# Optimization experiments

Measured on AMD Instinct MI355X. Metric: run time of the kernel, lower is better.

Reference implementation:

```python
import jax, jax.numpy as jnp
import numpy as np


def _conv_same(x, w):
    # NHWC input, HWIO kernel, stride 1, SAME padding
    return jax.lax.conv_general_dilated(
        x, w, window_strides=(1, 1), padding='SAME',
        dimension_numbers=('NHWC', 'HWIO', 'NHWC'))


def _maxpool2(x):
    return jax.lax.reduce_window(
        x, -jnp.inf, jax.lax.max,
        window_dimensions=(1, 2, 2, 1), window_strides=(1, 2, 2, 1),
        padding='VALID')


def _binarize(x):
    # sign binarization with straight-through estimator (XNOR-net / Riptide)
    return x + jax.lax.stop_gradient(jnp.sign(x) - x)


def _binary_conv_relu(x, w):
    # BinaryConv2D: binarize activations and weights, conv, relu, no bias
    return jax.nn.relu(_conv_same(_binarize(x), _binarize(w)))


def setup_inputs() -> dict:
    key = jax.random.key(0)
    ks = jax.random.split(key, 32)
    d = {}
    d['x'] = jax.random.normal(ks[0], (128, 32, 32, 3), dtype=jnp.float32)
    d['w1'] = jax.random.normal(ks[1], (3, 3, 3, 128), dtype=jnp.float32) * 0.1
    d['b1'] = jax.random.normal(ks[2], (128,), dtype=jnp.float32) * 0.1
    chans = [128, 128, 256, 256, 512, 512]
    kshapes = [(3, 3, 128, 128), (3, 3, 128, 256), (3, 3, 256, 256),
               (3, 3, 256, 512), (3, 3, 512, 512)]
    for i, shp in zip(range(2, 7), kshapes):
        d[f'w{i}'] = jax.random.normal(ks[2 + i], shp, dtype=jnp.float32) * 0.1
    for i in range(1, 7):
        c = chans[i - 1]
        d[f'bn{i}_scale'] = jax.random.uniform(ks[10 + i], (c,), dtype=jnp.float32, minval=0.5, maxval=1.5)
        d[f'bn{i}_bias'] = jax.random.normal(ks[20 + i], (c,), dtype=jnp.float32) * 0.1
    d['dense_w'] = jax.random.normal(ks[30], (512, 10), dtype=jnp.float32) * 0.05
    d['dense_b'] = jax.random.normal(ks[31], (10,), dtype=jnp.float32) * 0.05
    return d


def reference(x, w1, b1, bn1_scale, bn1_bias, w2, bn2_scale, bn2_bias,
              w3, bn3_scale, bn3_bias, w4, bn4_scale, bn4_bias,
              w5, bn5_scale, bn5_bias, w6, bn6_scale, bn6_bias,
              dense_w, dense_b):
    # conv1: normal float conv + relu, then BN (inference: fused scale/bias)
    h = jax.nn.relu(_conv_same(x, w1) + b1)
    h = h * bn1_scale + bn1_bias
    # conv2 (binary) -> pool -> bn2
    h = _binary_conv_relu(h, w2)
    h = _maxpool2(h)
    h = h * bn2_scale + bn2_bias
    # conv3 (binary) -> bn3
    h = _binary_conv_relu(h, w3)
    h = h * bn3_scale + bn3_bias
    # conv4 (binary) -> pool -> bn4
    h = _binary_conv_relu(h, w4)
    h = _maxpool2(h)
    h = h * bn4_scale + bn4_bias
    # conv5 (binary) -> bn5
    h = _binary_conv_relu(h, w5)
    h = h * bn5_scale + bn5_bias
    # conv6 (binary) -> pool -> bn6
    h = _binary_conv_relu(h, w6)
    h = _maxpool2(h)  # -> [B, 4, 4, 512]
    h = h * bn6_scale + bn6_bias
    # Dense applied on last axis (original code has no flatten): [B,4,4,10]
    logits = jnp.einsum('bhwc,cd->bhwd', h, dense_w) + dense_b
    return jax.nn.softmax(logits, axis=-1)
```

## Files before the change

### kernel.cpp

```cpp
#include <hip/hip_runtime.h>
#include <cstdint>
#include <math.h>

typedef unsigned long long u64;


__global__ void zero_kernel(u64* __restrict__ p, int n) {
    int i = blockIdx.x * blockDim.x + threadIdx.x;
    int stride = gridDim.x * blockDim.x;
    for (; i < n; i += stride) p[i] = 0;
}

__global__ __launch_bounds__(256) void pack_kernel(
        const float* __restrict__ w2, const float* __restrict__ w3,
        const float* __restrict__ w4, const float* __restrict__ w5,
        const float* __restrict__ w6,
        u64* __restrict__ wq2, u64* __restrict__ wq3, u64* __restrict__ wq4,
        u64* __restrict__ wq5, u64* __restrict__ wq6) {
    int wid = (blockIdx.x * 256 + threadIdx.x) >> 6;
    int lane = threadIdx.x & 63;
    const float* w; u64* wq; int Wi, Cout, base;
    if      (wid <  2304) { w = w2; wq = wq2; Wi = 2; Cout = 128; base = 0; }
    else if (wid <  6912) { w = w3; wq = wq3; Wi = 2; Cout = 256; base = 2304; }
    else if (wid < 16128) { w = w4; wq = wq4; Wi = 4; Cout = 256; base = 6912; }
    else if (wid < 34560) { w = w5; wq = wq5; Wi = 4; Cout = 512; base = 16128; }
    else if (wid < 71424) { w = w6; wq = wq6; Wi = 8; Cout = 512; base = 34560; }
    else return;
    int id = wid - base;
    int oc = id % Cout;
    int tw = id / Cout;
    int tap = tw / Wi, cw = tw % Wi;
    int Cin = Wi * 64;
    float v = w[((size_t)tap * Cin + cw * 64 + lane) * Cout + oc];
    u64 mask = __ballot(!(v > 0.0f));
    if (lane == 0) wq[((size_t)oc * Wi + cw) * 9 + tap] = mask;
}

__global__ __launch_bounds__(256) void meta_kernel(
        const u64* __restrict__ wq2, const u64* __restrict__ wq3,
        const u64* __restrict__ wq4, const u64* __restrict__ wq5,
        const u64* __restrict__ wq6,
        const float* s2, const float* b2, const float* s3, const float* b3,
        const float* s4, const float* b4, const float* s5, const float* b5,
        const float* s6, const float* b6,
        int* __restrict__ mt) {
    int wid = (blockIdx.x * 256 + threadIdx.x) >> 6;
    int lane = threadIdx.x & 63;
    if (wid >= 1664) return;
    const u64* wq; int WI, oc, mbase; const float* sc; const float* bi;
    if      (wid <  128) { wq = wq2; WI = 2; oc = wid;        mbase = 0;     sc = s2; bi = b2; }
    else if (wid <  384) { wq = wq3; WI = 2; oc = wid - 128;  mbase = 1536;  sc = s3; bi = b3; }
    else if (wid <  640) { wq = wq4; WI = 4; oc = wid - 384;  mbase = 4608;  sc = s4; bi = b4; }
    else if (wid < 1152) { wq = wq5; WI = 4; oc = wid - 640;  mbase = 7680;  sc = s5; bi = b5; }
    else                 { wq = wq6; WI = 8; oc = wid - 1152; mbase = 13824; sc = s6; bi = b6; }
    int P = 0;
    if (lane < 9) {
        int s = 0;
        for (int cw = 0; cw < WI; cw++)
            s += (int)__popcll(wq[((size_t)oc * WI + cw) * 9 + lane]);
        P = 64 * WI - s;
    }
    int p0 = __shfl(P, 0, 64), p1 = __shfl(P, 1, 64), p2 = __shfl(P, 2, 64);
    int p3 = __shfl(P, 3, 64), p5 = __shfl(P, 5, 64);
    int p6 = __shfl(P, 6, 64), p7 = __shfl(P, 7, 64), p8 = __shfl(P, 8, 64);
    if (lane == 0) {
        int* mo = mt + mbase + oc * 12;
        mo[0] = p0 + p1 + p2;
        mo[1] = p6 + p7 + p8;
        mo[2] = p0 + p3 + p6;
        mo[3] = p2 + p5 + p8;
        mo[4] = p0; mo[5] = p2; mo[6] = p6; mo[7] = p8;
        double tneg = -(double)bi[oc] / (double)sc[oc];
        mo[8] = (tneg < 0.0) ? -(1 << 29) : (int)floor(tneg);
    }
}

__global__ __launch_bounds__(128) void conv1_pack_kernel(
        const float* __restrict__ x, const float* __restrict__ w1,
        const float* __restrict__ b1, const float* __restrict__ s1,
        const float* __restrict__ bb1, u64* __restrict__ p1) {
    const int t = threadIdx.x;
    const int oc = t;
    const int bx = blockIdx.x;
    const int xseg = (bx & 3) << 3;
    const int y = (bx >> 2) & 31;
    const int b = bx >> 7;

    double wreg[27];
    #pragma unroll
    for (int k = 0; k < 27; k++) wreg[k] = (double)w1[k * 128 + oc];
    const double b1v = (double)b1[oc];
    const double tneg = -(double)bb1[oc] / (double)s1[oc];
    const bool always = tneg < 0.0;
    const double thr = tneg - b1v;

    double acc[8];
    #pragma unroll
    for (int i = 0; i < 8; i++) acc[i] = 0.0;

    #pragma unroll
    for (int ky = 0; ky < 3; ky++) {
        int iy = y - 1 + ky;
        if (iy < 0 || iy > 31) continue;
        #pragma unroll
        for (int col = 0; col < 10; col++) {
            int ix = xseg - 1 + col;
            if (ix < 0 || ix > 31) continue;
            const float* xp = x + ((b * 32 + iy) * 32 + ix) * 3;
            #pragma unroll
            for (int c = 0; c < 3; c++) {
                double xv = (double)xp[c];
                #pragma unroll
                for (int kx = 0; kx < 3; kx++) {
                    int px = col - kx;
                    if (px >= 0 && px < 8)
                        acc[px] += xv * wreg[(ky * 3 + kx) * 3 + c];
                }
            }
        }
    }
    const int w = t >> 6;
    #pragma unroll
    for (int px = 0; px < 8; px++) {
        bool bit = always || (acc[px] > thr);
        u64 m = __ballot(bit);
        if ((t & 63) == 0)
            p1[(((size_t)w * 128 + b) * 34 + y + 1) * 34 + xseg + px + 1] = m;
    }
}

template<int WI, int H, int W, int COUT, bool POOL, int OCG, bool BITOUT>
__global__ __launch_bounds__(256, 4) void bconv6_kernel(
        const u64* __restrict__ in, const u64* __restrict__ wq,
        const int* __restrict__ mt,
        const float* __restrict__ bns, const float* __restrict__ bnb,
        u64* __restrict__ outb, float* __restrict__ outf) {
    constexpr int Hp = H + 2, Wp = W + 2;
    constexpr int Ho = POOL ? H / 2 : H;
    constexpr int Wo = POOL ? W / 2 : W;
    constexpr int TX = W / 8;
    constexpr int TILES = (H / 8) * (W / 8);
    constexpr int NG = COUT / OCG;

    const int lane = threadIdx.x & 63;
    int wid = (blockIdx.x * blockDim.x + threadIdx.x) >> 6;
    wid = __builtin_amdgcn_readfirstlane(wid);
    const int g = wid % NG;
    int tb = wid / NG;
    const int tile = tb % TILES;
    const int b = tb / TILES;
    if (b >= 128) return;
    const int ly = lane >> 3, lx = lane & 7;
    const int py = (tile / TX) * 8 + ly;
    const int px = (tile % TX) * 8 + lx;
    const int oc0 = g * OCG;

    const int ft = (py == 0), fb = (py == H - 1);
    const int fl = (px == 0), fr = (px == W - 1);
    const int ctl = ft & fl, ctr = ft & fr, cbl = fb & fl, cbr = fb & fr;
    const int n_oob = 3 * (ft + fb + fl + fr) - ctl - ctr - cbl - cbr;
    const int dbase = -64 * WI * (9 + n_oob);
    const bool anyedge = __ballot(ft | fb | fl | fr) != 0;

    int m[OCG];
    #pragma unroll
    for (int o = 0; o < OCG; o++) m[o] = 0;

    const u64* ab = in + ((size_t)b * Hp + py) * Wp + px;
    const u64* wb0 = wq + (size_t)oc0 * WI * 9;

    #pragma unroll 1
    for (int cw = 0; cw < WI; cw++) {
        const u64* ap = ab + (size_t)cw * (128 * Hp * Wp);
        u64 act[9];
        #pragma unroll
        for (int ky = 0; ky < 3; ky++)
            #pragma unroll
            for (int kx = 0; kx < 3; kx++)
                act[ky * 3 + kx] = ap[ky * Wp + kx];
        const u64* wb = wb0 + (size_t)cw * 9;
        #pragma unroll
        for (int o = 0; o < OCG; o++) {
            const u64* wl = wb + (size_t)o * (WI * 9);
            int a0 = m[o], a1 = 0, a2 = 0, a3 = 0;
            #pragma unroll
            for (int t9 = 0; t9 < 9; t9++) {
                u64 xo = act[t9] ^ wl[t9];
                int lo = __builtin_popcount((unsigned)xo);
                int hi = __builtin_popcount((unsigned)(xo >> 32));
                if (t9 & 1) { a1 = lo + a1; a3 = hi + a3; }
                else        { a0 = lo + a0; a2 = hi + a2; }
            }
            m[o] = (a0 + a2) + (a1 + a3);
        }
    }

    const bool master = POOL ? (((ly | lx) & 1) == 0) : true;
    const int opy = POOL ? (py >> 1) : py, opx = POOL ? (px >> 1) : px;
    unsigned mask = 0;

    #pragma unroll
    for (int o = 0; o < OCG; o++) {
        const int* mo = mt + (size_t)(oc0 + o) * 12;
        int d;
        if (anyedge) {
            int S = ft * mo[0] + fb * mo[1] + fl * mo[2] + fr * mo[3]
                  - ctl * mo[4] - ctr * mo[5] - cbl * mo[6] - cbr * mo[7];
            d = 2 * (m[o] + S) + dbase;
        } else {
            d = 2 * m[o] - 64 * WI * 9;
        }
        if constexpr (BITOUT) {
            mask |= (unsigned)(d > mo[8]) << o;
        } else {
            int dm = max(d, __shfl_xor(d, 1, 64));
            int dp = max(dm, __shfl_xor(dm, 8, 64));
            int pmax = dp > 0 ? dp : 0;
            float h = (float)pmax * bns[oc0 + o] + bnb[oc0 + o];
            if (master)
                outf[(size_t)((b * 4 + opy) * 4 + opx) * 512 + oc0 + o] = h;
        }
    }

    if constexpr (BITOUT) {
        if constexpr (POOL) {
            mask |= __shfl_xor(mask, 1, 64);
            mask |= __shfl_xor(mask, 8, 64);
        }
        if (master) {
            size_t idx = (((size_t)(oc0 >> 6) * 128 + b) * (Ho + 2) + opy + 1)
                         * (Wo + 2) + opx + 1;
            char* bp = (char*)(outb + idx) + ((oc0 & 63) >> 3);
            if constexpr (OCG == 32) *(unsigned*)bp = mask;
            else *(unsigned short*)bp = (unsigned short)mask;
        }
    }
}

__global__ __launch_bounds__(256) void dense_softmax_kernel(
        const float* __restrict__ h6, const float* __restrict__ dw,
        const float* __restrict__ db, float* __restrict__ out) {
    int lane = threadIdx.x & 63;
    int r = (blockIdx.x * blockDim.x + threadIdx.x) >> 6;
    if (r >= 2048) return;
    const float* hr = h6 + (size_t)r * 512;
    float part[10];
    #pragma unroll
    for (int d = 0; d < 10; d++) part[d] = 0.f;
    #pragma unroll
    for (int k = 0; k < 8; k++) {
        int c = lane + 64 * k;
        float hv = hr[c];
        const float* dwr = dw + c * 10;
        #pragma unroll
        for (int d = 0; d < 10; d++) part[d] += hv * dwr[d];
    }
    #pragma unroll
    for (int off = 32; off >= 1; off >>= 1) {
        #pragma unroll
        for (int d = 0; d < 10; d++) part[d] += __shfl_down(part[d], off, 64);
    }
    if (lane == 0) {
        float logits[10];
        float mx = -1e30f;
        #pragma unroll
        for (int d = 0; d < 10; d++) { logits[d] = part[d] + db[d]; mx = fmaxf(mx, logits[d]); }
        float se = 0.f;
        #pragma unroll
        for (int d = 0; d < 10; d++) { logits[d] = expf(logits[d] - mx); se += logits[d]; }
        float inv = 1.f / se;
        #pragma unroll
        for (int d = 0; d < 10; d++) out[(size_t)r * 10 + d] = logits[d] * inv;
    }
}

extern "C" void kernel_launch(void* const* d_in, const int* in_sizes, int n_in,
                              void* d_out, int out_size, void* d_ws, size_t ws_size,
                              hipStream_t stream) {
    const float* x    = (const float*)d_in[0];
    const float* w1   = (const float*)d_in[1];
    const float* b1   = (const float*)d_in[2];
    const float* w2   = (const float*)d_in[3];
    const float* w3   = (const float*)d_in[4];
    const float* w4   = (const float*)d_in[5];
    const float* w5   = (const float*)d_in[6];
    const float* w6   = (const float*)d_in[7];
    const float* bn1s = (const float*)d_in[8];
    const float* bn1b = (const float*)d_in[9];
    const float* bn2s = (const float*)d_in[10];
    const float* bn2b = (const float*)d_in[11];
    const float* bn3s = (const float*)d_in[12];
    const float* bn3b = (const float*)d_in[13];
    const float* bn4s = (const float*)d_in[14];
    const float* bn4b = (const float*)d_in[15];
    const float* bn5s = (const float*)d_in[16];
    const float* bn5b = (const float*)d_in[17];
    const float* bn6s = (const float*)d_in[18];
    const float* bn6b = (const float*)d_in[19];
    const float* dw   = (const float*)d_in[20];
    const float* db   = (const float*)d_in[21];
    float* out = (float*)d_out;

    u64* ws   = (u64*)d_ws;
    u64* wq2  = ws;
    u64* wq3  = ws + 2304;
    u64* wq4  = ws + 6912;
    u64* wq5  = ws + 16128;
    u64* wq6  = ws + 34560;
    int* mt   = (int*)(ws + 71424);
    u64* p1   = ws + 81408;
    u64* p2   = ws + 377344;
    u64* p3   = ws + 460288;
    u64* p4   = ws + 626176;
    u64* p5   = ws + 677376;
    float* h6 = (float*)(ws + 779776);
    const int NPAD = 295936 + 82944 + 165888 + 51200 + 102400;

    int* mt2 = mt + 0;
    int* mt3 = mt + 1536;
    int* mt4 = mt + 4608;
    int* mt5 = mt + 7680;
    int* mt6 = mt + 13824;

    zero_kernel<<<1024, 256, 0, stream>>>(p1, NPAD);
    pack_kernel<<<17856, 256, 0, stream>>>(w2, w3, w4, w5, w6,
                                           wq2, wq3, wq4, wq5, wq6);
    meta_kernel<<<416, 256, 0, stream>>>(wq2, wq3, wq4, wq5, wq6,
        bn2s, bn2b, bn3s, bn3b, bn4s, bn4b, bn5s, bn5b, bn6s, bn6b, mt);

    conv1_pack_kernel<<<128*32*4, 128, 0, stream>>>(x, w1, b1, bn1s, bn1b, p1);

    bconv6_kernel<2,32,32,128,true, 32,true ><<<2048, 256, 0, stream>>>(p1, wq2, mt2, nullptr, nullptr, p2, nullptr);
    bconv6_kernel<2,16,16,256,false,32,true ><<<1024, 256, 0, stream>>>(p2, wq3, mt3, nullptr, nullptr, p3, nullptr);
    bconv6_kernel<4,16,16,256,true, 16,true ><<<2048, 256, 0, stream>>>(p3, wq4, mt4, nullptr, nullptr, p4, nullptr);
    bconv6_kernel<4,8,8,  512,false,16,true ><<<1024, 256, 0, stream>>>(p4, wq5, mt5, nullptr, nullptr, p5, nullptr);
    bconv6_kernel<8,8,8,  512,true, 16,false><<<1024, 256, 0, stream>>>(p5, wq6, mt6, bn6s, bn6b, nullptr, h6);

    dense_softmax_kernel<<<512, 256, 0, stream>>>(h6, dw, db, out);
}
```

Before: 354.8 us.

## Restructure binary conv to load multiple channel words before popcount over OC group

Replaces the per-channel-word loop with a chunked loop that loads up to four channel words of 3x3 activations via inline-asm batched global loads, then runs the XNOR-popcount over all output channels. The output-channel group is fixed at 16 for every layer, so the first two layers launch twice as many blocks. Launch bounds drop occupancy to 3 for the wider layers. The goal is to cut how often weights are refetched and to expose more memory-level parallelism. The cost is higher register pressure. The inline asm waits on vmcnt(0), which blocks the compiler from overlapping those loads with other work.

```diff
diff --git a/kernel.cpp b/kernel.cpp
--- a/kernel.cpp
+++ b/kernel.cpp
@@ -129,26 +129,80 @@
     }
 }
 
-template<int WI, int H, int W, int COUT, bool POOL, int OCG, bool BITOUT>
-__global__ __launch_bounds__(256, 4) void bconv6_kernel(
+__device__ __forceinline__ void vload9(
+        const u64* p0, const u64* p1, const u64* p2,
+        const u64* p3, const u64* p4, const u64* p5,
+        const u64* p6, const u64* p7, const u64* p8,
+        u64& a0, u64& a1, u64& a2, u64& a3, u64& a4,
+        u64& a5, u64& a6, u64& a7, u64& a8) {
+    asm volatile(
+        "global_load_dwordx2 %0, %9, off\n\t"
+        "global_load_dwordx2 %1, %10, off\n\t"
+        "global_load_dwordx2 %2, %11, off\n\t"
+        "global_load_dwordx2 %3, %12, off\n\t"
+        "global_load_dwordx2 %4, %13, off\n\t"
+        "global_load_dwordx2 %5, %14, off\n\t"
+        "global_load_dwordx2 %6, %15, off\n\t"
+        "global_load_dwordx2 %7, %16, off\n\t"
+        "global_load_dwordx2 %8, %17, off\n\t"
+        "s_waitcnt vmcnt(0)"
+        : "=&v"(a0), "=&v"(a1), "=&v"(a2), "=&v"(a3), "=&v"(a4),
+          "=&v"(a5), "=&v"(a6), "=&v"(a7), "=&v"(a8)
+        : "v"(p0), "v"(p1), "v"(p2), "v"(p3), "v"(p4),
+          "v"(p5), "v"(p6), "v"(p7), "v"(p8));
+}
+
+__device__ __forceinline__ int dot9(const u64* __restrict__ wl, const u64* A) {
+    int s0 = 0, s1 = 0, s2 = 0, s3 = 0;
+    u64 x;
+    x = A[0] ^ wl[0]; s0 = __builtin_popcount((unsigned)x) + s0; s2 = __builtin_popcount((unsigned)(x >> 32)) + s2;
+    x = A[1] ^ wl[1]; s1 = __builtin_popcount((unsigned)x) + s1; s3 = __builtin_popcount((unsigned)(x >> 32)) + s3;
+    x = A[2] ^ wl[2]; s0 = __builtin_popcount((unsigned)x) + s0; s2 = __builtin_popcount((unsigned)(x >> 32)) + s2;
+    x = A[3] ^ wl[3]; s1 = __builtin_popcount((unsigned)x) + s1; s3 = __builtin_popcount((unsigned)(x >> 32)) + s3;
+    x = A[4] ^ wl[4]; s0 = __builtin_popcount((unsigned)x) + s0; s2 = __builtin_popcount((unsigned)(x >> 32)) + s2;
+    x = A[5] ^ wl[5]; s1 = __builtin_popcount((unsigned)x) + s1; s3 = __builtin_popcount((unsigned)(x >> 32)) + s3;
+    x = A[6] ^ wl[6]; s0 = __builtin_popcount((unsigned)x) + s0; s2 = __builtin_popcount((unsigned)(x >> 32)) + s2;
+    x = A[7] ^ wl[7]; s1 = __builtin_popcount((unsigned)x) + s1; s3 = __builtin_popcount((unsigned)(x >> 32)) + s3;
+    x = A[8] ^ wl[8]; s0 = __builtin_popcount((unsigned)x) + s0; s2 = __builtin_popcount((unsigned)(x >> 32)) + s2;
+    return (s0 + s2) + (s1 + s3);
+}
+
+template<int OO, int OCG, int WI, int CHW>
+__device__ __forceinline__ void oc_rec(const u64* __restrict__ wb,
+                                       const u64* A, int* m) {
+    const u64* wl = wb + OO * (WI * 9);
+    int s = dot9(wl, A);
+    if constexpr (CHW > 1) s += dot9(wl + 9,  A + 9);
+    if constexpr (CHW > 2) s += dot9(wl + 18, A + 18);
+    if constexpr (CHW > 3) s += dot9(wl + 27, A + 27);
+    m[OO] += s;
+    if constexpr (OO + 1 < OCG) oc_rec<OO + 1, OCG, WI, CHW>(wb, A, m);
+}
+
+template<int WI, int H, int W, int COUT, bool POOL, bool BITOUT>
+__global__ __launch_bounds__(256, (WI >= 4) ? 3 : 4) void bconv8_kernel(
         const u64* __restrict__ in, const u64* __restrict__ wq,
         const int* __restrict__ mt,
         const float* __restrict__ bns, const float* __restrict__ bnb,
         u64* __restrict__ outb, float* __restrict__ outf) {
+    constexpr int OCG = 16;
     constexpr int Hp = H + 2, Wp = W + 2;
     constexpr int Ho = POOL ? H / 2 : H;
     constexpr int Wo = POOL ? W / 2 : W;
     constexpr int TX = W / 8;
-    constexpr int TILES = (H / 8) * (W / 8);
+    constexpr int TPI = (H / 8) * (W / 8);
     constexpr int NG = COUT / OCG;
+    constexpr int CHW = (WI < 4) ? WI : 4;
+    constexpr int NCH = WI / CHW;
+    const size_t PS = (size_t)128 * Hp * Wp;
 
     const int lane = threadIdx.x & 63;
     int wid = (blockIdx.x * blockDim.x + threadIdx.x) >> 6;
     wid = __builtin_amdgcn_readfirstlane(wid);
     const int g = wid % NG;
     int tb = wid / NG;
-    const int tile = tb % TILES;
-    const int b = tb / TILES;
+    const int tile = tb % TPI;
+    const int b = tb / TPI;
     if (b >= 128) return;
     const int ly = lane >> 3, lx = lane & 7;
     const int py = (tile / TX) * 8 + ly;
@@ -162,77 +216,81 @@
     const int dbase = -64 * WI * (9 + n_oob);
     const bool anyedge = __ballot(ft | fb | fl | fr) != 0;
 
-    int m[OCG];
-    #pragma unroll
-    for (int o = 0; o < OCG; o++) m[o] = 0;
-
     const u64* ab = in + ((size_t)b * Hp + py) * Wp + px;
     const u64* wb0 = wq + (size_t)oc0 * WI * 9;
 
+    int m[OCG];
+    #pragma unroll
+    for (int i = 0; i < OCG; i++) m[i] = 0;
+
     #pragma unroll 1
-    for (int cw = 0; cw < WI; cw++) {
-        const u64* ap = ab + (size_t)cw * (128 * Hp * Wp);
-        u64 act[9];
-        #pragma unroll
-        for (int ky = 0; ky < 3; ky++)
-            #pragma unroll
-            for (int kx = 0; kx < 3; kx++)
-                act[ky * 3 + kx] = ap[ky * Wp + kx];
-        const u64* wb = wb0 + (size_t)cw * 9;
-        #pragma unroll
-        for (int o = 0; o < OCG; o++) {
-            const u64* wl = wb + (size_t)o * (WI * 9);
-            int a0 = m[o], a1 = 0, a2 = 0, a3 = 0;
-            #pragma unroll
-            for (int t9 = 0; t9 < 9; t9++) {
-                u64 xo = act[t9] ^ wl[t9];
-                int lo = __builtin_popcount((unsigned)xo);
-                int hi = __builtin_popcount((unsigned)(xo >> 32));
-                if (t9 & 1) { a1 = lo + a1; a3 = hi + a3; }
-                else        { a0 = lo + a0; a2 = hi + a2; }
-            }
-            m[o] = (a0 + a2) + (a1 + a3);
-        }
+    for (int cb = 0; cb < NCH; ++cb) {
+        u64 A[CHW * 9];
+        {
+            const u64* ap = ab + (size_t)(cb * CHW) * PS;
+            vload9(ap, ap + 1, ap + 2, ap + Wp, ap + Wp + 1, ap + Wp + 2,
+                   ap + 2 * Wp, ap + 2 * Wp + 1, ap + 2 * Wp + 2,
+                   A[0], A[1], A[2], A[3], A[4], A[5], A[6], A[7], A[8]);
+        }
+        if constexpr (CHW > 1) {
+            const u64* ap = ab + (size_t)(cb * CHW + 1) * PS;
+            vload9(ap, ap + 1, ap + 2, ap + Wp, ap + Wp + 1, ap + Wp + 2,
+                   ap + 2 * Wp, ap + 2 * Wp + 1, ap + 2 * Wp + 2,
+                   A[9], A[10], A[11], A[12], A[13], A[14], A[15], A[16], A[17]);
+        }
+        if constexpr (CHW > 2) {
+            const u64* ap = ab + (size_t)(cb * CHW + 2) * PS;
+            vload9(ap, ap + 1, ap + 2, ap + Wp, ap + Wp + 1, ap + Wp + 2,
+                   ap + 2 * Wp, ap + 2 * Wp + 1, ap + 2 * Wp + 2,
+                   A[18], A[19], A[20], A[21], A[22], A[23], A[24], A[25], A[26]);
+        }
+        if constexpr (CHW > 3) {
+            const u64* ap = ab + (size_t)(cb * CHW + 3) * PS;
+            vload9(ap, ap + 1, ap + 2, ap + Wp, ap + Wp + 1, ap + Wp + 2,
+                   ap + 2 * Wp, ap + 2 * Wp + 1, ap + 2 * Wp + 2,
+                   A[27], A[28], A[29], A[30], A[31], A[32], A[33], A[34], A[35]);
+        }
+        oc_rec<0, OCG, WI, CHW>(wb0 + cb * CHW * 9, A, m);
     }
 
     const bool master = POOL ? (((ly | lx) & 1) == 0) : true;
     const int opy = POOL ? (py >> 1) : py, opx = POOL ? (px >> 1) : px;
-    unsigned mask = 0;
-
-    #pragma unroll
-    for (int o = 0; o < OCG; o++) {
-        const int* mo = mt + (size_t)(oc0 + o) * 12;
+    unsigned omask = 0;
+
+    #pragma unroll
+    for (int oo = 0; oo < OCG; oo++) {
+        const int* mo = mt + (size_t)(oc0 + oo) * 12;
         int d;
         if (anyedge) {
             int S = ft * mo[0] + fb * mo[1] + fl * mo[2] + fr * mo[3]
                   - ctl * mo[4] - ctr * mo[5] - cbl * mo[6] - cbr * mo[7];
-            d = 2 * (m[o] + S) + dbase;
+            d = 2 * (m[oo] + S) + dbase;
         } else {
-            d = 2 * m[o] - 64 * WI * 9;
+            d = 2 * m[oo] - 64 * WI * 9;
         }
         if constexpr (BITOUT) {
-            mask |= (unsigned)(d > mo[8]) << o;
+            omask |= (unsigned)(d > mo[8]) << oo;
         } else {
             int dm = max(d, __shfl_xor(d, 1, 64));
             int dp = max(dm, __shfl_xor(dm, 8, 64));
             int pmax = dp > 0 ? dp : 0;
-            float h = (float)pmax * bns[oc0 + o] + bnb[oc0 + o];
+            const int oc = oc0 + oo;
+            float h = (float)pmax * bns[oc] + bnb[oc];
             if (master)
-                outf[(size_t)((b * 4 + opy) * 4 + opx) * 512 + oc0 + o] = h;
+                outf[(size_t)((b * 4 + opy) * 4 + opx) * 512 + oc] = h;
         }
     }
 
     if constexpr (BITOUT) {
         if constexpr (POOL) {
-            mask |= __shfl_xor(mask, 1, 64);
-            mask |= __shfl_xor(mask, 8, 64);
+            omask |= __shfl_xor(omask, 1, 64);
+            omask |= __shfl_xor(omask, 8, 64);
         }
         if (master) {
             size_t idx = (((size_t)(oc0 >> 6) * 128 + b) * (Ho + 2) + opy + 1)
                          * (Wo + 2) + opx + 1;
             char* bp = (char*)(outb + idx) + ((oc0 & 63) >> 3);
-            if constexpr (OCG == 32) *(unsigned*)bp = mask;
-            else *(unsigned short*)bp = (unsigned short)mask;
+            *(unsigned short*)bp = (unsigned short)omask;
         }
     }
 }
@@ -330,11 +388,11 @@
 
     conv1_pack_kernel<<<128*32*4, 128, 0, stream>>>(x, w1, b1, bn1s, bn1b, p1);
 
-    bconv6_kernel<2,32,32,128,true, 32,true ><<<2048, 256, 0, stream>>>(p1, wq2, mt2, nullptr, nullptr, p2, nullptr);
-    bconv6_kernel<2,16,16,256,false,32,true ><<<1024, 256, 0, stream>>>(p2, wq3, mt3, nullptr, nullptr, p3, nullptr);
-    bconv6_kernel<4,16,16,256,true, 16,true ><<<2048, 256, 0, stream>>>(p3, wq4, mt4, nullptr, nullptr, p4, nullptr);
-    bconv6_kernel<4,8,8,  512,false,16,true ><<<1024, 256, 0, stream>>>(p4, wq5, mt5, nullptr, nullptr, p5, nullptr);
-    bconv6_kernel<8,8,8,  512,true, 16,false><<<1024, 256, 0, stream>>>(p5, wq6, mt6, bn6s, bn6b, nullptr, h6);
+    bconv8_kernel<2,32,32,128,true, true ><<<4096, 256, 0, stream>>>(p1, wq2, mt2, nullptr, nullptr, p2, nullptr);
+    bconv8_kernel<2,16,16,256,false,true ><<<2048, 256, 0, stream>>>(p2, wq3, mt3, nullptr, nullptr, p3, nullptr);
+    bconv8_kernel<4,16,16,256,true, true ><<<2048, 256, 0, stream>>>(p3, wq4, mt4, nullptr, nullptr, p4, nullptr);
+    bconv8_kernel<4,8,8,  512,false,true ><<<1024, 256, 0, stream>>>(p4, wq5, mt5, nullptr, nullptr, p5, nullptr);
+    bconv8_kernel<8,8,8,  512,true, false><<<1024, 256, 0, stream>>>(p5, wq6, mt6, bn6s, bn6b, nullptr, h6);
 
     dense_softmax_kernel<<<512, 256, 0, stream>>>(h6, dw, db, out);
 }
```

Measured after the change: 646.4 us. +82.2%, slower.
